# Kernel optimization log

Measured on AMD Instinct MI355X. Metric: run time of the kernel, lower is better.

The kernel has to match this reference:

```python
import jax, jax.numpy as jnp
import numpy as np


def setup_inputs() -> dict:
    key = jax.random.key(0)
    ks = jax.random.split(key, 7)
    B, T, D, H, O = 64, 512, 256, 1024, 256
    s = 0.02  # small init scale for numerical stability of the recurrence
    return {
        "x": jax.random.normal(ks[0], (B, T, D), dtype=jnp.float32),
        "W_ih": jax.random.normal(ks[1], (4 * H, D), dtype=jnp.float32) * s,
        "W_hh": jax.random.normal(ks[2], (4 * H, H), dtype=jnp.float32) * s,
        "b_ih": jax.random.normal(ks[3], (4 * H,), dtype=jnp.float32) * s,
        "b_hh": jax.random.normal(ks[4], (4 * H,), dtype=jnp.float32) * s,
        "W_out": jax.random.normal(ks[5], (O, H), dtype=jnp.float32) * s,
        "b_out": jax.random.normal(ks[6], (O,), dtype=jnp.float32) * s,
    }


def reference(x, W_ih, W_hh, b_ih, b_hh, W_out, b_out):
    # x: [B, T, D]. Faithful to torch nn.LSTMCell gate order (i, f, g, o)
    # followed by a per-step Linear projection, future=0 path.
    B, T, D = x.shape
    H = W_hh.shape[1]

    # Precompute input contributions for all timesteps in one GEMM: [T, B, 4H]
    xg = jnp.einsum('btd,gd->tbg', x, W_ih) + b_ih + b_hh

    def step(carry, xg_t):
        h, c = carry
        gates = xg_t + h @ W_hh.T  # [B, 4H]
        i, f, g, o = jnp.split(gates, 4, axis=-1)
        i = jax.nn.sigmoid(i)
        f = jax.nn.sigmoid(f)
        g = jnp.tanh(g)
        o = jax.nn.sigmoid(o)
        c = f * c + i * g
        h = o * jnp.tanh(c)
        return (h, c), h

    h0 = jnp.zeros((B, H), dtype=x.dtype)
    c0 = jnp.zeros((B, H), dtype=x.dtype)
    _, hs = jax.lax.scan(step, (h0, c0), xg)  # hs: [T, B, H]

    # Per-step Linear, batched over time: [B, T, O]
    outputs = jnp.einsum('tbh,oh->bto', hs, W_out) + b_out
    return outputs
```

## Files before the change

### kernel.cpp

```cpp
#include <hip/hip_runtime.h>

#define B_ 64
#define T_ 512
#define D_ 256
#define H_ 1024
#define O_ 256
#define KTOT 1280
#define NBLK 256

typedef __bf16 bf16x8 __attribute__((ext_vector_type(8)));
typedef float f32x4 __attribute__((ext_vector_type(4)));

__device__ __forceinline__ unsigned short f2bf(float f) {
    unsigned int u = __builtin_bit_cast(unsigned int, f);
    unsigned int r = (u + 0x7fffu + ((u >> 16) & 1u)) >> 16;
    return (unsigned short)r;
}
__device__ __forceinline__ float sigmoid_f(float x) { return 1.f / (1.f + __expf(-x)); }
__device__ __forceinline__ float tanh_f(float x)    { return 1.f - 2.f / (1.f + __expf(2.f * x)); }

#define SYNC_INTS 540672

__global__ void zero_sync(int* s) { s[blockIdx.x * 256 + threadIdx.x] = 0; }

__global__ __launch_bounds__(256) void pack_weights(
    const float* __restrict__ Wih, const float* __restrict__ Whh,
    const float* __restrict__ bih, const float* __restrict__ bhh,
    const float* __restrict__ Wout,
    unsigned short* __restrict__ Wp, float* __restrict__ bpk,
    unsigned short* __restrict__ Wo)
{
    int bid = blockIdx.x, tid = threadIdx.x;
    if (bid < 4096) {
        int g = bid & 3, j = (bid >> 2) & 3, hc = (bid >> 4) * 4 + j;
        int row = g * 1024 + hc;
        for (int e = tid; e < KTOT; e += 256) {
            float v = (e < D_) ? Wih[(size_t)row * D_ + e] : Whh[(size_t)row * H_ + (e - D_)];
            Wp[(size_t)bid * KTOT + e] = f2bf(v);
        }
        if (tid == 0) bpk[bid] = bih[row] + bhh[row];
    } else {
        int r = bid - 4096;
        for (int e = tid; e < H_; e += 256)
            Wo[(size_t)r * H_ + e] = f2bf(Wout[(size_t)r * H_ + e]);
    }
}

__global__ __launch_bounds__(256) void x_pack(const float* __restrict__ x,
                                              unsigned short* __restrict__ xt)
{
    int bid = blockIdx.x;
    int b = bid >> 9, t = bid & 511;
    int d = threadIdx.x;
    xt[((size_t)t * B_ + b) * D_ + d] = f2bf(x[(size_t)bid * D_ + d]);
}

__global__ __launch_bounds__(256, 1) void lstm_scan(
    const unsigned short* __restrict__ Wp, const float* __restrict__ bpk,
    const unsigned short* __restrict__ xt, unsigned short* __restrict__ hs,
    int* __restrict__ sync)
{
    const int tid  = threadIdx.x;
    const int wid  = tid >> 6, lane = tid & 63;
    const int n    = lane & 15, kg = lane >> 4;
    const int blk  = blockIdx.x;
    const int gq   = n & 3;
    const int hcol = blk * 4 + (n >> 2);

    bf16x8 wf[40];
    {
        const bf16x8* wp8 = (const bf16x8*)(Wp + (size_t)(blk * 16 + n) * KTOT + kg * 8);
        #pragma unroll
        for (int kk = 0; kk < 40; ++kk) wf[kk] = wp8[kk * 4];
    }
    #pragma unroll
    for (int kk = 0; kk < 40; ++kk) asm volatile("" : "+v"(wf[kk]));

    const float bias = bpk[blk * 16 + n];

    float cc[4] = {0.f, 0.f, 0.f, 0.f};

    for (int t = 0; t < T_; ++t) {
        f32x4 ac[4];
        f32x4 z = {0.f, 0.f, 0.f, 0.f};
        ac[0] = z; ac[1] = z; ac[2] = z; ac[3] = z;

        {
            const bf16x8* ax = (const bf16x8*)(xt + ((size_t)t * B_ + wid * 16 + n) * D_ + kg * 8);
            #pragma unroll
            for (int kk = 0; kk < 8; ++kk) {
                bf16x8 a = ax[kk * 4];
                ac[kk & 3] = __builtin_amdgcn_mfma_f32_16x16x32_bf16(a, wf[kk], ac[kk & 3], 0, 0, 0);
            }
        }

        if (t > 0) {
            if (tid == 0) {
                while (__hip_atomic_load(sync + (278528 + ((t - 1) * 16 + (blk & 15)) * 32),
                                         __ATOMIC_RELAXED, __HIP_MEMORY_SCOPE_AGENT) == 0) {
                    __builtin_amdgcn_s_sleep(1);
                }
            }
            __syncthreads();
            const bf16x8* ah = (const bf16x8*)(hs + ((size_t)(t - 1) * B_ + wid * 16 + n) * H_ + kg * 8);
            #pragma unroll
            for (int kk = 8; kk < 40; ++kk) {
                bf16x8 a = ah[(kk - 8) * 4];
                ac[kk & 3] = __builtin_amdgcn_mfma_f32_16x16x32_bf16(a, wf[kk], ac[kk & 3], 0, 0, 0);
            }
        }

        f32x4 g4 = (ac[0] + ac[1]) + (ac[2] + ac[3]);

        float hv[4];
        #pragma unroll
        for (int r = 0; r < 4; ++r) {
            float v  = g4[r] + bias;
            float v1 = __shfl_xor(v, 1);
            float v2 = __shfl_xor(v, 2);
            float v3 = __shfl_xor(v, 3);
            float iv = (gq == 0) ? v  : (gq == 1) ? v1 : (gq == 2) ? v2 : v3;
            float fv = (gq == 0) ? v1 : (gq == 1) ? v  : (gq == 2) ? v3 : v2;
            float gv = (gq == 0) ? v2 : (gq == 1) ? v3 : (gq == 2) ? v  : v1;
            float ov = (gq == 0) ? v3 : (gq == 1) ? v2 : (gq == 2) ? v1 : v;
            float is = sigmoid_f(iv), fs = sigmoid_f(fv), gt = tanh_f(gv), os = sigmoid_f(ov);
            float cn = fs * cc[r] + is * gt;
            cc[r] = cn;
            hv[r] = os * tanh_f(cn);
        }

        if (gq == 0) {
            #pragma unroll
            for (int r = 0; r < 4; ++r) {
                int br = wid * 16 + kg * 4 + r;
                __hip_atomic_store(hs + ((size_t)t * B_ + br) * H_ + hcol, f2bf(hv[r]),
                                   __ATOMIC_RELAXED, __HIP_MEMORY_SCOPE_AGENT);
            }
        }

        __syncthreads();
        if (tid == 0) {
            int lf = __hip_atomic_fetch_add(sync + ((t * 16 + (blk >> 4)) * 32), 1,
                                            __ATOMIC_RELAXED, __HIP_MEMORY_SCOPE_AGENT);
            if (lf == 15) {
                int rt = __hip_atomic_fetch_add(sync + (262144 + t * 32), 1,
                                                __ATOMIC_RELAXED, __HIP_MEMORY_SCOPE_AGENT);
                if (rt == 15) {
                    #pragma unroll
                    for (int i = 0; i < 16; ++i)
                        __hip_atomic_store(sync + (278528 + (t * 16 + i) * 32), 1,
                                           __ATOMIC_RELAXED, __HIP_MEMORY_SCOPE_AGENT);
                }
            }
        }
    }
}

__global__ __launch_bounds__(256) void out_proj(
    const unsigned short* __restrict__ hs, const unsigned short* __restrict__ Wo,
    const float* __restrict__ bout, float* __restrict__ out)
{
    const int tid = threadIdx.x, wid = tid >> 6, lane = tid & 63;
    const int n = lane & 15, kg = lane >> 4;
    const int mb = blockIdx.x >> 2, nb = blockIdx.x & 3;
    const int m0 = mb * 64 + wid * 16;
    const int n0 = nb * 64;
    f32x4 acc[4];
    f32x4 z = {0.f, 0.f, 0.f, 0.f};
    acc[0] = z; acc[1] = z; acc[2] = z; acc[3] = z;
    const bf16x8* ap = (const bf16x8*)(hs + ((size_t)(m0 + n)) * H_ + kg * 8);
    #pragma unroll 2
    for (int kk = 0; kk < 32; ++kk) {
        bf16x8 a = ap[kk * 4];
        #pragma unroll
        for (int nt = 0; nt < 4; ++nt) {
            const bf16x8* bp8 = (const bf16x8*)(Wo + ((size_t)(n0 + nt * 16 + n)) * H_ + kg * 8);
            bf16x8 b = bp8[kk * 4];
            acc[nt] = __builtin_amdgcn_mfma_f32_16x16x32_bf16(a, b, acc[nt], 0, 0, 0);
        }
    }
    #pragma unroll
    for (int nt = 0; nt < 4; ++nt) {
        int col = n0 + nt * 16 + n;
        float bias = bout[col];
        #pragma unroll
        for (int r = 0; r < 4; ++r) {
            int m = m0 + kg * 4 + r;
            int tt = m >> 6, bb = m & 63;
            out[((size_t)bb * T_ + tt) * O_ + col] = acc[nt][r] + bias;
        }
    }
}

extern "C" void kernel_launch(void* const* d_in, const int* in_sizes, int n_in,
                              void* d_out, int out_size, void* d_ws, size_t ws_size,
                              hipStream_t stream)
{
    const float* x    = (const float*)d_in[0];
    const float* Wih  = (const float*)d_in[1];
    const float* Whh  = (const float*)d_in[2];
    const float* bih  = (const float*)d_in[3];
    const float* bhh  = (const float*)d_in[4];
    const float* Wout = (const float*)d_in[5];
    const float* bout = (const float*)d_in[6];
    float* out = (float*)d_out;

    char* ws = (char*)d_ws;
    unsigned short* Wp  = (unsigned short*)ws;  ws += (size_t)4096 * KTOT * 2;
    float*          bpk = (float*)ws;           ws += (size_t)4096 * 4;
    unsigned short* Wo  = (unsigned short*)ws;  ws += (size_t)O_ * H_ * 2;
    unsigned short* xt  = (unsigned short*)ws;  ws += (size_t)T_ * B_ * D_ * 2;
    unsigned short* hs  = (unsigned short*)ws;  ws += (size_t)T_ * B_ * H_ * 2;
    int*            syn = (int*)ws;             ws += (size_t)SYNC_INTS * 4;

    if (ws_size < (size_t)(ws - (char*)d_ws)) return;

    zero_sync<<<SYNC_INTS / 256, 256, 0, stream>>>(syn);
    pack_weights<<<4096 + 256, 256, 0, stream>>>(Wih, Whh, bih, bhh, Wout, Wp, bpk, Wo);
    x_pack<<<B_ * T_, 256, 0, stream>>>(x, xt);

    {
        const unsigned short* Wpc = Wp;
        const float*          bpc = bpk;
        const unsigned short* xtc = xt;
        unsigned short*       hsv = hs;
        int*                  syv = syn;
        void* args[5] = {(void*)&Wpc, (void*)&bpc, (void*)&xtc, (void*)&hsv, (void*)&syv};
        hipLaunchCooperativeKernel((void*)lstm_scan, dim3(NBLK), dim3(256), args, 0, stream);
    }

    out_proj<<<(T_ * B_ / 64) * 4, 256, 0, stream>>>(hs, Wo, bout, out);
}
```

Baseline: 4.242 ms.

## Halve scan blocks, stage h tiles in LDS, use per-block flags

The persistent LSTM scan now runs on 128 blocks of 512 threads instead of 256 blocks of 256, so each block owns 32 packed gate columns (8 hidden units) and the weight packing order changes to match. Each block gathers its new h values in shared memory and writes them out as 16-byte rows per batch element, replacing scattered 2-byte atomic stores. The hierarchical fetch-add barrier becomes one flag per block per step, which a full wavefront polls with vector loads. The aim is fewer grid-barrier round trips and fewer store transactions per timestep. The cost is more work per block and the loss of the tree reduction, so every block now reads all 128 flags.

```diff
diff --git a/kernel.cpp b/kernel.cpp
--- a/kernel.cpp
+++ b/kernel.cpp
@@ -6,7 +6,8 @@
 #define H_ 1024
 #define O_ 256
 #define KTOT 1280
-#define NBLK 256
+#define NBLK 128
+#define NTHR 512
 
 typedef __bf16 bf16x8 __attribute__((ext_vector_type(8)));
 typedef float f32x4 __attribute__((ext_vector_type(4)));
@@ -19,7 +20,7 @@
 __device__ __forceinline__ float sigmoid_f(float x) { return 1.f / (1.f + __expf(-x)); }
 __device__ __forceinline__ float tanh_f(float x)    { return 1.f - 2.f / (1.f + __expf(2.f * x)); }
 
-#define SYNC_INTS 540672
+#define SYNC_INTS (T_ * NBLK)
 
 __global__ void zero_sync(int* s) { s[blockIdx.x * 256 + threadIdx.x] = 0; }
 
@@ -32,7 +33,7 @@
 {
     int bid = blockIdx.x, tid = threadIdx.x;
     if (bid < 4096) {
-        int g = bid & 3, j = (bid >> 2) & 3, hc = (bid >> 4) * 4 + j;
+        int g = bid & 3, hc = bid >> 2;
         int row = g * 1024 + hc;
         for (int e = tid; e < KTOT; e += 256) {
             float v = (e < D_) ? Wih[(size_t)row * D_ + e] : Whh[(size_t)row * H_ + (e - D_)];
@@ -55,28 +56,32 @@
     xt[((size_t)t * B_ + b) * D_ + d] = f2bf(x[(size_t)bid * D_ + d]);
 }
 
-__global__ __launch_bounds__(256, 1) void lstm_scan(
+__global__ __launch_bounds__(NTHR, 2) void lstm_scan(
     const unsigned short* __restrict__ Wp, const float* __restrict__ bpk,
     const unsigned short* __restrict__ xt, unsigned short* __restrict__ hs,
     int* __restrict__ sync)
 {
     const int tid  = threadIdx.x;
-    const int wid  = tid >> 6, lane = tid & 63;
+    const int w    = tid >> 6, lane = tid & 63;
     const int n    = lane & 15, kg = lane >> 4;
     const int blk  = blockIdx.x;
+    const int mt   = w >> 1, nt = w & 1;
+    const int m0   = mt * 16;
     const int gq   = n & 3;
-    const int hcol = blk * 4 + (n >> 2);
+    const int pc   = blk * 32 + nt * 16 + n;
+
+    __shared__ unsigned short hbuf[64][8];
 
     bf16x8 wf[40];
     {
-        const bf16x8* wp8 = (const bf16x8*)(Wp + (size_t)(blk * 16 + n) * KTOT + kg * 8);
+        const bf16x8* wp8 = (const bf16x8*)(Wp + (size_t)pc * KTOT + kg * 8);
         #pragma unroll
         for (int kk = 0; kk < 40; ++kk) wf[kk] = wp8[kk * 4];
     }
     #pragma unroll
     for (int kk = 0; kk < 40; ++kk) asm volatile("" : "+v"(wf[kk]));
 
-    const float bias = bpk[blk * 16 + n];
+    const float bias = bpk[pc];
 
     float cc[4] = {0.f, 0.f, 0.f, 0.f};
 
@@ -86,7 +91,7 @@
         ac[0] = z; ac[1] = z; ac[2] = z; ac[3] = z;
 
         {
-            const bf16x8* ax = (const bf16x8*)(xt + ((size_t)t * B_ + wid * 16 + n) * D_ + kg * 8);
+            const bf16x8* ax = (const bf16x8*)(xt + ((size_t)t * B_ + m0 + n) * D_ + kg * 8);
             #pragma unroll
             for (int kk = 0; kk < 8; ++kk) {
                 bf16x8 a = ax[kk * 4];
@@ -95,14 +100,17 @@
         }
 
         if (t > 0) {
-            if (tid == 0) {
-                while (__hip_atomic_load(sync + (278528 + ((t - 1) * 16 + (blk & 15)) * 32),
-                                         __ATOMIC_RELAXED, __HIP_MEMORY_SCOPE_AGENT) == 0) {
+            if (w == 0) {
+                const int* fl = sync + (size_t)(t - 1) * NBLK;
+                for (;;) {
+                    int v0 = __hip_atomic_load(fl + lane,      __ATOMIC_RELAXED, __HIP_MEMORY_SCOPE_AGENT);
+                    int v1 = __hip_atomic_load(fl + lane + 64, __ATOMIC_RELAXED, __HIP_MEMORY_SCOPE_AGENT);
+                    if (__all((v0 != 0) && (v1 != 0))) break;
                     __builtin_amdgcn_s_sleep(1);
                 }
             }
             __syncthreads();
-            const bf16x8* ah = (const bf16x8*)(hs + ((size_t)(t - 1) * B_ + wid * 16 + n) * H_ + kg * 8);
+            const bf16x8* ah = (const bf16x8*)(hs + ((size_t)(t - 1) * B_ + m0 + n) * H_ + kg * 8);
             #pragma unroll
             for (int kk = 8; kk < 40; ++kk) {
                 bf16x8 a = ah[(kk - 8) * 4];
@@ -130,28 +138,24 @@
         }
 
         if (gq == 0) {
+            int colL = nt * 4 + (n >> 2);
             #pragma unroll
-            for (int r = 0; r < 4; ++r) {
-                int br = wid * 16 + kg * 4 + r;
-                __hip_atomic_store(hs + ((size_t)t * B_ + br) * H_ + hcol, f2bf(hv[r]),
+            for (int r = 0; r < 4; ++r)
+                hbuf[m0 + kg * 4 + r][colL] = f2bf(hv[r]);
+        }
+
+        __syncthreads();
+
+        if (w == 0) {
+            const unsigned long long* hb = (const unsigned long long*)&hbuf[lane][0];
+            unsigned long long v0 = hb[0], v1 = hb[1];
+            unsigned long long* dst = (unsigned long long*)(hs + ((size_t)t * B_ + lane) * H_ + blk * 8);
+            __hip_atomic_store(dst,     v0, __ATOMIC_RELAXED, __HIP_MEMORY_SCOPE_AGENT);
+            __hip_atomic_store(dst + 1, v1, __ATOMIC_RELAXED, __HIP_MEMORY_SCOPE_AGENT);
+            asm volatile("s_waitcnt vmcnt(0)" ::: "memory");
+            if (lane == 0)
+                __hip_atomic_store(sync + (size_t)t * NBLK + blk, 1,
                                    __ATOMIC_RELAXED, __HIP_MEMORY_SCOPE_AGENT);
-            }
-        }
-
-        __syncthreads();
-        if (tid == 0) {
-            int lf = __hip_atomic_fetch_add(sync + ((t * 16 + (blk >> 4)) * 32), 1,
-                                            __ATOMIC_RELAXED, __HIP_MEMORY_SCOPE_AGENT);
-            if (lf == 15) {
-                int rt = __hip_atomic_fetch_add(sync + (262144 + t * 32), 1,
-                                                __ATOMIC_RELAXED, __HIP_MEMORY_SCOPE_AGENT);
-                if (rt == 15) {
-                    #pragma unroll
-                    for (int i = 0; i < 16; ++i)
-                        __hip_atomic_store(sync + (278528 + (t * 16 + i) * 32), 1,
-                                           __ATOMIC_RELAXED, __HIP_MEMORY_SCOPE_AGENT);
-                }
-            }
         }
     }
 }
@@ -226,7 +230,7 @@
         unsigned short*       hsv = hs;
         int*                  syv = syn;
         void* args[5] = {(void*)&Wpc, (void*)&bpc, (void*)&xtc, (void*)&hsv, (void*)&syv};
-        hipLaunchCooperativeKernel((void*)lstm_scan, dim3(NBLK), dim3(256), args, 0, stream);
+        hipLaunchCooperativeKernel((void*)lstm_scan, dim3(NBLK), dim3(NTHR), args, 0, stream);
     }
 
     out_proj<<<(T_ * B_ / 64) * 4, 256, 0, stream>>>(hs, Wo, bout, out);
```

Measured after the change: 5.790 ms. +36.5%, slower.

## Replace hierarchical atomic barrier with per-block arrival flags and rotating master release

Applied to the files above, without the earlier changes.

The two-level fetch-add counter tree is replaced by per-block arrival flags for each timestep. A master block that rotates with the timestep polls all 256 flags with one wavefront and then sets 8 release flags. Every wavefront spins on a release flag itself, which removes the thread-0 wait, the sleep and the __syncthreads before the recurrent GEMM. The goal is lower grid-barrier latency on the serial 512-step chain, at the cost of heavier polling traffic and a per-step master whose own wait adds to its critical path.

```diff
diff --git a/kernel.cpp b/kernel.cpp
--- a/kernel.cpp
+++ b/kernel.cpp
@@ -7,6 +7,7 @@
 #define O_ 256
 #define KTOT 1280
 #define NBLK 256
+#define NTHR 256
 
 typedef __bf16 bf16x8 __attribute__((ext_vector_type(8)));
 typedef float f32x4 __attribute__((ext_vector_type(4)));
@@ -19,7 +20,9 @@
 __device__ __forceinline__ float sigmoid_f(float x) { return 1.f / (1.f + __expf(-x)); }
 __device__ __forceinline__ float tanh_f(float x)    { return 1.f - 2.f / (1.f + __expf(2.f * x)); }
 
-#define SYNC_INTS 540672
+#define ARR_OFF 0
+#define RLS_OFF (T_ * NBLK)
+#define SYNC_INTS (T_ * NBLK + T_ * 128)
 
 __global__ void zero_sync(int* s) { s[blockIdx.x * 256 + threadIdx.x] = 0; }
 
@@ -55,17 +58,18 @@
     xt[((size_t)t * B_ + b) * D_ + d] = f2bf(x[(size_t)bid * D_ + d]);
 }
 
-__global__ __launch_bounds__(256, 1) void lstm_scan(
+__global__ __launch_bounds__(NTHR, 1) void lstm_scan(
     const unsigned short* __restrict__ Wp, const float* __restrict__ bpk,
     const unsigned short* __restrict__ xt, unsigned short* __restrict__ hs,
     int* __restrict__ sync)
 {
     const int tid  = threadIdx.x;
-    const int wid  = tid >> 6, lane = tid & 63;
+    const int w    = tid >> 6, lane = tid & 63;
+    const int blk  = blockIdx.x;
     const int n    = lane & 15, kg = lane >> 4;
-    const int blk  = blockIdx.x;
     const int gq   = n & 3;
     const int hcol = blk * 4 + (n >> 2);
+    const int m0   = w * 16;
 
     bf16x8 wf[40];
     {
@@ -86,7 +90,7 @@
         ac[0] = z; ac[1] = z; ac[2] = z; ac[3] = z;
 
         {
-            const bf16x8* ax = (const bf16x8*)(xt + ((size_t)t * B_ + wid * 16 + n) * D_ + kg * 8);
+            const bf16x8* ax = (const bf16x8*)(xt + ((size_t)t * B_ + m0 + n) * D_ + kg * 8);
             #pragma unroll
             for (int kk = 0; kk < 8; ++kk) {
                 bf16x8 a = ax[kk * 4];
@@ -95,14 +99,13 @@
         }
 
         if (t > 0) {
-            if (tid == 0) {
-                while (__hip_atomic_load(sync + (278528 + ((t - 1) * 16 + (blk & 15)) * 32),
-                                         __ATOMIC_RELAXED, __HIP_MEMORY_SCOPE_AGENT) == 0) {
-                    __builtin_amdgcn_s_sleep(1);
-                }
-            }
-            __syncthreads();
-            const bf16x8* ah = (const bf16x8*)(hs + ((size_t)(t - 1) * B_ + wid * 16 + n) * H_ + kg * 8);
+            const bool selfrel = (w == 0) && (blk == ((t - 1) & (NBLK - 1)));
+            if (!selfrel) {
+                const int* rw = sync + RLS_OFF + (size_t)(t - 1) * 128 + (((blk << 2) + w) & 7) * 16;
+                while (__hip_atomic_load(rw, __ATOMIC_RELAXED, __HIP_MEMORY_SCOPE_AGENT) == 0) {}
+            }
+
+            const bf16x8* ah = (const bf16x8*)(hs + ((size_t)(t - 1) * B_ + m0 + n) * H_ + kg * 8);
             #pragma unroll
             for (int kk = 8; kk < 40; ++kk) {
                 bf16x8 a = ah[(kk - 8) * 4];
@@ -132,26 +135,33 @@
         if (gq == 0) {
             #pragma unroll
             for (int r = 0; r < 4; ++r) {
-                int br = wid * 16 + kg * 4 + r;
+                int br = m0 + kg * 4 + r;
                 __hip_atomic_store(hs + ((size_t)t * B_ + br) * H_ + hcol, f2bf(hv[r]),
                                    __ATOMIC_RELAXED, __HIP_MEMORY_SCOPE_AGENT);
             }
         }
-
+        asm volatile("s_waitcnt vmcnt(0)" ::: "memory");
         __syncthreads();
-        if (tid == 0) {
-            int lf = __hip_atomic_fetch_add(sync + ((t * 16 + (blk >> 4)) * 32), 1,
-                                            __ATOMIC_RELAXED, __HIP_MEMORY_SCOPE_AGENT);
-            if (lf == 15) {
-                int rt = __hip_atomic_fetch_add(sync + (262144 + t * 32), 1,
-                                                __ATOMIC_RELAXED, __HIP_MEMORY_SCOPE_AGENT);
-                if (rt == 15) {
-                    #pragma unroll
-                    for (int i = 0; i < 16; ++i)
-                        __hip_atomic_store(sync + (278528 + (t * 16 + i) * 32), 1,
-                                           __ATOMIC_RELAXED, __HIP_MEMORY_SCOPE_AGENT);
+
+        if (tid == 0)
+            __hip_atomic_store(sync + ARR_OFF + (size_t)t * NBLK + blk, 1,
+                               __ATOMIC_RELAXED, __HIP_MEMORY_SCOPE_AGENT);
+
+        if ((w == 0) && (blk == (t & (NBLK - 1))) && (t < T_ - 1)) {
+            const int* ap = sync + ARR_OFF + (size_t)t * NBLK + lane * 4;
+            for (;;) {
+                int ok = 1;
+                #pragma unroll
+                for (int j = 0; j < 4; ++j) {
+                    int idx = lane * 4 + j;
+                    ok &= (idx == blk) |
+                          (__hip_atomic_load(ap + j, __ATOMIC_RELAXED, __HIP_MEMORY_SCOPE_AGENT) != 0);
                 }
-            }
+                if (__all(ok)) break;
+            }
+            if (lane < 8)
+                __hip_atomic_store(sync + RLS_OFF + (size_t)t * 128 + lane * 16, 1,
+                                   __ATOMIC_RELAXED, __HIP_MEMORY_SCOPE_AGENT);
         }
     }
 }
@@ -226,7 +236,7 @@
         unsigned short*       hsv = hs;
         int*                  syv = syn;
         void* args[5] = {(void*)&Wpc, (void*)&bpc, (void*)&xtc, (void*)&hsv, (void*)&syv};
-        hipLaunchCooperativeKernel((void*)lstm_scan, dim3(NBLK), dim3(256), args, 0, stream);
+        hipLaunchCooperativeKernel((void*)lstm_scan, dim3(NBLK), dim3(NTHR), args, 0, stream);
     }
 
     out_proj<<<(T_ * B_ / 64) * 4, 256, 0, stream>>>(hs, Wo, bout, out);
```

Measured after the change: 4.285 ms. About the same (+1.0%).
